# Optimization experiments

Hardware: AMD Instinct MI355X
Metric: run time of the kernel (lower is better)

The kernel has to match this reference:

```python
import jax, jax.numpy as jnp
import numpy as np

BETA = 0.45
GAMMA = 0.45
EPS = 1e-12  # F.normalize eps

N_PRED = 16384
N_GT = 32768


def setup_inputs() -> dict:
    key = jax.random.key(0)
    k1, k2, k3, k4 = jax.random.split(key, 4)
    pred_feat = jax.random.normal(k1, (N_PRED, 6), dtype=jnp.float32)
    gt_data = jax.random.normal(k2, (N_GT, 6), dtype=jnp.float32)
    R = jax.random.normal(k3, (3, 3), dtype=jnp.float32)
    t = jax.random.normal(k4, (3,), dtype=jnp.float32)
    s = jnp.ones((1,), dtype=jnp.float32)
    return {"pred_feat": pred_feat, "gt_data": gt_data, "R": R, "t": t, "s": s}


def _l2_normalize(x):
    # matches F.normalize(p=2, dim=1, eps=1e-12): x / max(||x||, eps)
    n = jnp.linalg.norm(x, axis=-1, keepdims=True)
    return x / jnp.maximum(n, EPS)


def reference(pred_feat, gt_data, R, t, s):
    # --- registration loss (R,t,s come from the external TEASER++ solver) ---
    I = jnp.eye(3, dtype=R.dtype)
    rot_loss = jnp.linalg.norm(R - I)          # Frobenius norm
    trans_loss = jnp.linalg.norm(t)            # L2 norm
    scale_loss = (s[0] - 1.0) ** 2
    reg_loss = rot_loss + trans_loss + scale_loss

    # --- nearest-neighbor normal loss ---
    pred_points = pred_feat[:, :3]   # [N,3]
    pred_normals = pred_feat[:, 3:]  # [N,3]
    gt_points = gt_data[:, :3]       # [L,3]
    gt_normals = gt_data[:, 3:]      # [L,3]

    # squared euclidean distances [N,L]; argmin identical to cdist argmin
    p2 = jnp.sum(pred_points * pred_points, axis=1, keepdims=True)  # [N,1]
    g2 = jnp.sum(gt_points * gt_points, axis=1)                     # [L]
    d2 = p2 + g2[None, :] - 2.0 * (pred_points @ gt_points.T)       # [N,L]
    min_indices = jnp.argmin(d2, axis=1)                            # [N]

    closest_gt_normals = gt_normals[min_indices]                    # [N,3]
    pred_u = _l2_normalize(pred_normals)
    gt_u = _l2_normalize(closest_gt_normals)
    cos_theta = jnp.sum(pred_u * gt_u, axis=1)
    norm_loss = jnp.mean(1.0 - cos_theta)

    return BETA * reg_loss + GAMMA * norm_loss
```

## Files before the change

### kernel.cpp

```cpp
#include <hip/hip_runtime.h>
#include <math.h>

#define NPRED 16384
#define NGT   32768
#define BETA  0.45f
#define GAMMA 0.45f

#define NGROUP 16
#define SPG    4
#define GSPLIT (NGROUP * SPG)
#define NTILE  (NGT / 32)
#define TPS    (NTILE / GSPLIT)
#define PB     256
#define NN_BX  (NPRED / PB)
#define RESB   (NPRED / 8)

typedef float f32x16 __attribute__((ext_vector_type(16)));
typedef short short8 __attribute__((ext_vector_type(8)));

__device__ __forceinline__ unsigned bf16h(float f) {
    unsigned u = __float_as_uint(f);
    return (u + 0x7FFFu + ((u >> 16) & 1u)) >> 16;
}
__device__ __forceinline__ float bf16f(unsigned h) { return __uint_as_float(h << 16); }
__device__ __forceinline__ unsigned pk2(unsigned lo, unsigned hi) { return lo | (hi << 16); }

#define MFMA_V(D, A, B, ZC)                                                    \
    asm("v_mfma_f32_32x32x16_bf16 %0, %1, %2, %3"                              \
        : "=&v"(D) : "v"(A), "v"(B), "v"(ZC))

__device__ __forceinline__ float tile_key3(const f32x16 acc, float vmask, int gtile) {
    float m0, m1, m2, m3, m4, n0, n1, key;
    asm("v_min3_f32 %0, %1, %2, %3" : "=v"(m0) : "v"(acc[0]),  "v"(acc[1]),  "v"(acc[2]));
    asm("v_min3_f32 %0, %1, %2, %3" : "=v"(m1) : "v"(acc[3]),  "v"(acc[4]),  "v"(acc[5]));
    asm("v_min3_f32 %0, %1, %2, %3" : "=v"(m2) : "v"(acc[6]),  "v"(acc[7]),  "v"(acc[8]));
    asm("v_min3_f32 %0, %1, %2, %3" : "=v"(m3) : "v"(acc[9]),  "v"(acc[10]), "v"(acc[11]));
    asm("v_min3_f32 %0, %1, %2, %3" : "=v"(m4) : "v"(acc[12]), "v"(acc[13]), "v"(acc[14]));
    asm("v_min3_f32 %0, %1, %2, %3" : "=v"(n0) : "v"(m0), "v"(m1), "v"(m2));
    asm("v_min3_f32 %0, %1, %2, %3" : "=v"(n1) : "v"(m3), "v"(m4), "v"(acc[15]));
    asm("v_min_f32 %0, %1, %2"      : "=v"(key) : "v"(n0), "v"(n1));
    asm("v_and_or_b32 %0, %1, %2, %3" : "+v"(key) : "v"(vmask), "s"(gtile));
    return key;
}

__device__ __forceinline__ void conv_row(float x, float y, float z,
                                         uint4* __restrict__ buf, int lrow) {
    const float g2 = fmaf(x, x, fmaf(y, y, z * z));
    const unsigned xh = bf16h(x),  yh = bf16h(y),  zh = bf16h(z),  gh = bf16h(g2);
    const unsigned xl = bf16h(x - bf16f(xh)), yl = bf16h(y - bf16f(yh));
    const unsigned zl = bf16h(z - bf16f(zh)), gl = bf16h(g2 - bf16f(gh));
    const int tl = lrow >> 5, r = lrow & 31;
    buf[tl * 64 + r]      = make_uint4(pk2(xh, xh), pk2(xl, xl), pk2(yh, yh), pk2(yl, yl));
    buf[tl * 64 + 32 + r] = make_uint4(pk2(zh, zh), pk2(zl, zl), pk2(gh, gl), 0u);
}

__global__ __launch_bounds__(256, 4) void nn_kernel(
    const float* __restrict__ pred,
    const float* __restrict__ gt,
    unsigned* __restrict__ packed2)
{
    __shared__ uint4 AF[2][TPS * 64];

    const int l  = threadIdx.x & 63;
    const int w  = threadIdx.x >> 6;

    const int pbase = blockIdx.x * PB + w * 64;
    const int c     = l & 31;
    const bool hi   = l >= 32;
    uint4 bu0, bu1;
    {
        const int pi = pbase + c;
        const float x = pred[pi * 6 + 0], y = pred[pi * 6 + 1], zc = pred[pi * 6 + 2];
        const float mx = -2.0f * x, my = -2.0f * y, mz = -2.0f * zc;
        const unsigned xh = bf16h(mx), yh = bf16h(my), zh = bf16h(mz);
        const unsigned xl = bf16h(mx - bf16f(xh)), yl = bf16h(my - bf16f(yh));
        const unsigned zl = bf16h(mz - bf16f(zh));
        bu0.x = hi ? pk2(zh, zl) : pk2(xh, xl);
        bu0.y = bu0.x;
        bu0.z = hi ? 0x3F803F80u : pk2(yh, yl);
        bu0.w = hi ? 0u : bu0.z;
    }
    {
        const int pi = pbase + 32 + c;
        const float x = pred[pi * 6 + 0], y = pred[pi * 6 + 1], zc = pred[pi * 6 + 2];
        const float mx = -2.0f * x, my = -2.0f * y, mz = -2.0f * zc;
        const unsigned xh = bf16h(mx), yh = bf16h(my), zh = bf16h(mz);
        const unsigned xl = bf16h(mx - bf16f(xh)), yl = bf16h(my - bf16f(yh));
        const unsigned zl = bf16h(mz - bf16f(zh));
        bu1.x = hi ? pk2(zh, zl) : pk2(xh, xl);
        bu1.y = bu1.x;
        bu1.z = hi ? 0x3F803F80u : pk2(yh, yl);
        bu1.w = hi ? 0u : bu1.z;
    }
    const short8 bv0 = *(const short8*)&bu0;
    const short8 bv1 = *(const short8*)&bu1;
    const f32x16 zacc = {0.f,0.f,0.f,0.f,0.f,0.f,0.f,0.f,
                         0.f,0.f,0.f,0.f,0.f,0.f,0.f,0.f};
    const float vmask = __uint_as_float(0xFFFFFC00u);

    float kmin0 = 1e30f, kmin1 = 1e30f;
    const int sp0 = blockIdx.y * SPG;

    float2 r0a, r0b, r1a, r1b;
    {
        const int j0 = sp0 * 512 + threadIdx.x;
        const float2* p0 = (const float2*)(gt + j0 * 6);
        const float2* p1 = (const float2*)(gt + (j0 + 256) * 6);
        r0a = p0[0]; r0b = p0[1];
        r1a = p1[0]; r1b = p1[1];
    }
    conv_row(r0a.x, r0a.y, r0b.x, AF[0], threadIdx.x);
    conv_row(r1a.x, r1a.y, r1b.x, AF[0], threadIdx.x + 256);
    __syncthreads();

#pragma unroll 1
    for (int u = 0; u < SPG; ++u) {
        const int sp = sp0 + u;
        uint4* cur = AF[u & 1];
        uint4* nxt = AF[(u + 1) & 1];
        const bool more = (u + 1 < SPG);

        if (more) {
            const int j0 = (sp + 1) * 512 + threadIdx.x;
            const float2* p0 = (const float2*)(gt + j0 * 6);
            const float2* p1 = (const float2*)(gt + (j0 + 256) * 6);
            r0a = p0[0]; r0b = p0[1];
            r1a = p1[0]; r1b = p1[1];
        }

        const int t0 = sp * TPS;
#pragma unroll 1
        for (int tt = 0; tt < TPS; tt += 2) {
            const uint4 aua = cur[tt * 64 + l];
            const uint4 aub = cur[(tt + 1) * 64 + l];
            const short8 ava = *(const short8*)&aua;
            const short8 avb = *(const short8*)&aub;
            const int ga = t0 + tt, gb = t0 + tt + 1;

            f32x16 acc_a0, acc_b0, acc_a1, acc_b1;
            MFMA_V(acc_a0, ava, bv0, zacc);
            MFMA_V(acc_b0, avb, bv0, zacc);
            const float ka0 = tile_key3(acc_a0, vmask, ga);
            MFMA_V(acc_a1, ava, bv1, zacc);
            const float kb0 = tile_key3(acc_b0, vmask, gb);
            MFMA_V(acc_b1, avb, bv1, zacc);
            asm("v_min3_f32 %0, %0, %1, %2" : "+v"(kmin0) : "v"(ka0), "v"(kb0));
            const float ka1 = tile_key3(acc_a1, vmask, ga);
            const float kb1 = tile_key3(acc_b1, vmask, gb);
            asm("v_min3_f32 %0, %0, %1, %2" : "+v"(kmin1) : "v"(ka1), "v"(kb1));
        }

        if (more) {
            conv_row(r0a.x, r0a.y, r0b.x, nxt, threadIdx.x);
            conv_row(r1a.x, r1a.y, r1b.x, nxt, threadIdx.x + 256);
        }
        __syncthreads();
    }

    kmin0 = fminf(kmin0, __shfl_xor(kmin0, 32, 64));
    kmin1 = fminf(kmin1, __shfl_xor(kmin1, 32, 64));

    const float km = hi ? kmin1 : kmin0;
    packed2[(size_t)(pbase + l) * NGROUP + blockIdx.y] = __float_as_uint(km);
}

__global__ __launch_bounds__(256) void rescan_kernel(
    const float* __restrict__ pred,
    const float* __restrict__ gt,
    const unsigned* __restrict__ packed2,
    float* __restrict__ partials)
{
    __shared__ float part[8];
    const int w = threadIdx.x >> 6, l = threadIdx.x & 63;
    const int half = l >> 5, jl = l & 31;
    const int pi = blockIdx.x * 8 + w * 2 + half;

    const unsigned* kp = packed2 + (size_t)pi * NGROUP;
    float e = (jl < NGROUP) ? __uint_as_float(kp[jl]) : 1e30f;
#pragma unroll
    for (int off = 16; off; off >>= 1)
        e = fminf(e, __shfl_xor(e, off, 32));
    const unsigned tix = __float_as_uint(e) & 0x3FFu;

    const int row = (int)tix * 32 + jl;
    const float2* gr = (const float2*)(gt + row * 6);
    const float2 ga = gr[0], gb = gr[1];
    const float gx = ga.x, gy = ga.y, gz = gb.x;
    const float g2 = fmaf(gx, gx, fmaf(gy, gy, gz * gz));
    const float2* pr = (const float2*)(pred + pi * 6);
    const float2 pa = pr[0], pb = pr[1];
    const float px = pa.x, py = pa.y, pz = pb.x;
    float d = fmaf(px, -2.0f * gx, fmaf(py, -2.0f * gy, fmaf(pz, -2.0f * gz, g2)));
    int jj = jl;
#pragma unroll
    for (int off = 16; off; off >>= 1) {
        const float d2 = __shfl_xor(d, off, 32);
        const int   j2 = __shfl_xor(jj, off, 32);
        const bool t = (d2 < d) || (d2 == d && j2 < jj);
        d  = t ? d2 : d;
        jj = t ? j2 : jj;
    }
    if (jl == 0) {
        const int idx = (int)tix * 32 + jj;
        const float nx = pred[pi * 6 + 3], ny = pred[pi * 6 + 4], nz = pred[pi * 6 + 5];
        const float ax = gt[idx * 6 + 3],  ay = gt[idx * 6 + 4],  az = gt[idx * 6 + 5];
        const float pn = fmaxf(sqrtf(fmaf(nx, nx, fmaf(ny, ny, nz * nz))), 1e-12f);
        const float gn = fmaxf(sqrtf(fmaf(ax, ax, fmaf(ay, ay, az * az))), 1e-12f);
        part[w * 2 + half] = 1.0f - fmaf(nx, ax, fmaf(ny, ay, nz * az)) / (pn * gn);
    }
    __syncthreads();
    if (threadIdx.x == 0) {
        float s = 0.f;
#pragma unroll
        for (int i = 0; i < 8; ++i) s += part[i];
        partials[blockIdx.x] = s;
    }
}

__global__ __launch_bounds__(256) void final_kernel(
    const float* __restrict__ partials,
    const float* __restrict__ Rm,
    const float* __restrict__ tv,
    const float* __restrict__ sv,
    float* __restrict__ out)
{
    __shared__ float ws_[4];
    float s = 0.f;
    for (int i = threadIdx.x; i < RESB; i += 256) s += partials[i];
#pragma unroll
    for (int off = 32; off; off >>= 1) s += __shfl_down(s, off, 64);
    if ((threadIdx.x & 63) == 0) ws_[threadIdx.x >> 6] = s;
    __syncthreads();
    if (threadIdx.x == 0) {
        const float t = ws_[0] + ws_[1] + ws_[2] + ws_[3];
        float rs = 0.f;
#pragma unroll
        for (int k = 0; k < 9; ++k) {
            const float v = Rm[k] - ((k % 4 == 0) ? 1.0f : 0.0f);
            rs = fmaf(v, v, rs);
        }
        const float rot = sqrtf(rs);
        const float tr  = sqrtf(fmaf(tv[0], tv[0], fmaf(tv[1], tv[1], tv[2] * tv[2])));
        const float sc  = (sv[0] - 1.0f) * (sv[0] - 1.0f);
        out[0] = GAMMA * t / (float)NPRED + BETA * (rot + tr + sc);
    }
}

extern "C" void kernel_launch(void* const* d_in, const int* in_sizes, int n_in,
                              void* d_out, int out_size, void* d_ws, size_t ws_size,
                              hipStream_t stream)
{
    const float* pred = (const float*)d_in[0];
    const float* gt   = (const float*)d_in[1];
    const float* Rm   = (const float*)d_in[2];
    const float* tv   = (const float*)d_in[3];
    const float* sv   = (const float*)d_in[4];
    float* out = (float*)d_out;

    unsigned* packed2 = (unsigned*)d_ws;
    float* partials   = (float*)((char*)d_ws + (size_t)NPRED * NGROUP * 4);

    nn_kernel<<<dim3(NN_BX, NGROUP), 256, 0, stream>>>(pred, gt, packed2);
    rescan_kernel<<<RESB, 256, 0, stream>>>(pred, gt, packed2, partials);
    final_kernel<<<1, 256, 0, stream>>>(partials, Rm, tv, sv, out);
}
```

Measured before the change: 33.81 us.

## Precompute bf16 GT tiles in prep kernel and stage via global_load_lds

```diff
diff --git a/kernel.cpp b/kernel.cpp
--- a/kernel.cpp
+++ b/kernel.cpp
@@ -6,11 +6,11 @@
 #define BETA  0.45f
 #define GAMMA 0.45f
 
-#define NGROUP 16
+#define NGROUP 32
 #define SPG    4
 #define GSPLIT (NGROUP * SPG)
 #define NTILE  (NGT / 32)
-#define TPS    (NTILE / GSPLIT)
+#define TPS    8
 #define PB     256
 #define NN_BX  (NPRED / PB)
 #define RESB   (NPRED / 8)
@@ -25,9 +25,9 @@
 __device__ __forceinline__ float bf16f(unsigned h) { return __uint_as_float(h << 16); }
 __device__ __forceinline__ unsigned pk2(unsigned lo, unsigned hi) { return lo | (hi << 16); }
 
-#define MFMA_V(D, A, B, ZC)                                                    \
-    asm("v_mfma_f32_32x32x16_bf16 %0, %1, %2, %3"                              \
-        : "=&v"(D) : "v"(A), "v"(B), "v"(ZC))
+#define MFMA0(D, A, B)                                                         \
+    asm("v_mfma_f32_32x32x16_bf16 %0, %1, %2, 0"                               \
+        : "=&v"(D) : "v"(A), "v"(B))
 
 __device__ __forceinline__ float tile_key3(const f32x16 acc, float vmask, int gtile) {
     float m0, m1, m2, m3, m4, n0, n1, key;
@@ -43,20 +43,29 @@
     return key;
 }
 
-__device__ __forceinline__ void conv_row(float x, float y, float z,
-                                         uint4* __restrict__ buf, int lrow) {
+__device__ __forceinline__ void gload_lds16(const uint4* g, uint4* l) {
+    __builtin_amdgcn_global_load_lds(
+        (const __attribute__((address_space(1))) void*)g,
+        (__attribute__((address_space(3))) void*)l, 16, 0, 0);
+}
+
+__global__ __launch_bounds__(256) void prep_kernel(
+    const float* __restrict__ gt, uint4* __restrict__ AFg)
+{
+    const int j = blockIdx.x * 256 + threadIdx.x;
+    const float x = gt[j * 6 + 0], y = gt[j * 6 + 1], z = gt[j * 6 + 2];
     const float g2 = fmaf(x, x, fmaf(y, y, z * z));
     const unsigned xh = bf16h(x),  yh = bf16h(y),  zh = bf16h(z),  gh = bf16h(g2);
     const unsigned xl = bf16h(x - bf16f(xh)), yl = bf16h(y - bf16f(yh));
     const unsigned zl = bf16h(z - bf16f(zh)), gl = bf16h(g2 - bf16f(gh));
-    const int tl = lrow >> 5, r = lrow & 31;
-    buf[tl * 64 + r]      = make_uint4(pk2(xh, xh), pk2(xl, xl), pk2(yh, yh), pk2(yl, yl));
-    buf[tl * 64 + 32 + r] = make_uint4(pk2(zh, zh), pk2(zl, zl), pk2(gh, gl), 0u);
-}
-
-__global__ __launch_bounds__(256, 4) void nn_kernel(
+    const int tile = j >> 5, r = j & 31;
+    AFg[tile * 64 + r]      = make_uint4(pk2(xh, xh), pk2(xl, xl), pk2(yh, yh), pk2(yl, yl));
+    AFg[tile * 64 + 32 + r] = make_uint4(pk2(zh, zh), pk2(zl, zl), pk2(gh, gl), 0u);
+}
+
+__global__ __launch_bounds__(256, 8) void nn_kernel(
     const float* __restrict__ pred,
-    const float* __restrict__ gt,
+    const uint4* __restrict__ AFg,
     unsigned* __restrict__ packed2)
 {
     __shared__ uint4 AF[2][TPS * 64];
@@ -94,23 +103,20 @@
     }
     const short8 bv0 = *(const short8*)&bu0;
     const short8 bv1 = *(const short8*)&bu1;
-    const f32x16 zacc = {0.f,0.f,0.f,0.f,0.f,0.f,0.f,0.f,
-                         0.f,0.f,0.f,0.f,0.f,0.f,0.f,0.f};
     const float vmask = __uint_as_float(0xFFFFFC00u);
 
     float kmin0 = 1e30f, kmin1 = 1e30f;
     const int sp0 = blockIdx.y * SPG;
 
-    float2 r0a, r0b, r1a, r1b;
-    {
-        const int j0 = sp0 * 512 + threadIdx.x;
-        const float2* p0 = (const float2*)(gt + j0 * 6);
-        const float2* p1 = (const float2*)(gt + (j0 + 256) * 6);
-        r0a = p0[0]; r0b = p0[1];
-        r1a = p1[0]; r1b = p1[1];
-    }
-    conv_row(r0a.x, r0a.y, r0b.x, AF[0], threadIdx.x);
-    conv_row(r1a.x, r1a.y, r1b.x, AF[0], threadIdx.x + 256);
+#define STAGE(BUF, SP)                                                         \
+    {                                                                          \
+        const uint4* src = AFg + (size_t)(SP) * (TPS * 64) + w * 128 + l;      \
+        gload_lds16(src,      &BUF[w * 128]);                                  \
+        gload_lds16(src + 64, &BUF[w * 128 + 64]);                             \
+    }
+
+    STAGE(AF[0], sp0)
+    asm volatile("s_waitcnt vmcnt(0)" ::: "memory");
     __syncthreads();
 
 #pragma unroll 1
@@ -118,15 +124,8 @@
         const int sp = sp0 + u;
         uint4* cur = AF[u & 1];
         uint4* nxt = AF[(u + 1) & 1];
-        const bool more = (u + 1 < SPG);
-
-        if (more) {
-            const int j0 = (sp + 1) * 512 + threadIdx.x;
-            const float2* p0 = (const float2*)(gt + j0 * 6);
-            const float2* p1 = (const float2*)(gt + (j0 + 256) * 6);
-            r0a = p0[0]; r0b = p0[1];
-            r1a = p1[0]; r1b = p1[1];
-        }
+
+        if (u + 1 < SPG) STAGE(nxt, sp + 1)
 
         const int t0 = sp * TPS;
 #pragma unroll 1
@@ -137,25 +136,23 @@
             const short8 avb = *(const short8*)&aub;
             const int ga = t0 + tt, gb = t0 + tt + 1;
 
-            f32x16 acc_a0, acc_b0, acc_a1, acc_b1;
-            MFMA_V(acc_a0, ava, bv0, zacc);
-            MFMA_V(acc_b0, avb, bv0, zacc);
-            const float ka0 = tile_key3(acc_a0, vmask, ga);
-            MFMA_V(acc_a1, ava, bv1, zacc);
-            const float kb0 = tile_key3(acc_b0, vmask, gb);
-            MFMA_V(acc_b1, avb, bv1, zacc);
+            f32x16 a0, b0, a1, b1;
+            MFMA0(a0, ava, bv0);
+            MFMA0(b0, avb, bv0);
+            const float ka0 = tile_key3(a0, vmask, ga);
+            MFMA0(a1, ava, bv1);
+            const float kb0 = tile_key3(b0, vmask, gb);
+            MFMA0(b1, avb, bv1);
             asm("v_min3_f32 %0, %0, %1, %2" : "+v"(kmin0) : "v"(ka0), "v"(kb0));
-            const float ka1 = tile_key3(acc_a1, vmask, ga);
-            const float kb1 = tile_key3(acc_b1, vmask, gb);
+            const float ka1 = tile_key3(a1, vmask, ga);
+            const float kb1 = tile_key3(b1, vmask, gb);
             asm("v_min3_f32 %0, %0, %1, %2" : "+v"(kmin1) : "v"(ka1), "v"(kb1));
         }
 
-        if (more) {
-            conv_row(r0a.x, r0a.y, r0b.x, nxt, threadIdx.x);
-            conv_row(r1a.x, r1a.y, r1b.x, nxt, threadIdx.x + 256);
-        }
+        asm volatile("s_waitcnt vmcnt(0)" ::: "memory");
         __syncthreads();
     }
+#undef STAGE
 
     kmin0 = fminf(kmin0, __shfl_xor(kmin0, 32, 64));
     kmin1 = fminf(kmin1, __shfl_xor(kmin1, 32, 64));
@@ -176,7 +173,7 @@
     const int pi = blockIdx.x * 8 + w * 2 + half;
 
     const unsigned* kp = packed2 + (size_t)pi * NGROUP;
-    float e = (jl < NGROUP) ? __uint_as_float(kp[jl]) : 1e30f;
+    float e = __uint_as_float(kp[jl]);
 #pragma unroll
     for (int off = 16; off; off >>= 1)
         e = fminf(e, __shfl_xor(e, off, 32));
@@ -259,8 +256,10 @@
 
     unsigned* packed2 = (unsigned*)d_ws;
     float* partials   = (float*)((char*)d_ws + (size_t)NPRED * NGROUP * 4);
-
-    nn_kernel<<<dim3(NN_BX, NGROUP), 256, 0, stream>>>(pred, gt, packed2);
+    uint4* AFg = (uint4*)((char*)d_ws + (size_t)NPRED * NGROUP * 4 + 16384);
+
+    prep_kernel<<<NGT / 256, 256, 0, stream>>>(gt, AFg);
+    nn_kernel<<<dim3(NN_BX, NGROUP), 256, 0, stream>>>(pred, AFg, packed2);
     rescan_kernel<<<RESB, 256, 0, stream>>>(pred, gt, packed2, partials);
     final_kernel<<<1, 256, 0, stream>>>(partials, Rm, tv, sv, out);
 }
```

New measurement: 36.47 us. +7.9%, slower.
